# Kernel tuning notes

Hardware: AMD Instinct MI355X
Metric: run time of the kernel (lower is better)

The kernel has to match this reference:

```python
import jax, jax.numpy as jnp
import numpy as np

V, E, H, L, B = 32004, 512, 512, 128, 64  # vocab(+4), emb, hidden, seq_len, batch


def setup_inputs() -> dict:
    key = jax.random.key(0)
    ks = jax.random.split(key, 8)
    emb = jax.random.normal(ks[0], (V, E), jnp.float32) * 0.02
    emb = emb.at[0].set(0.0)  # padding_idx = PAD = 0
    Wx_f = jax.random.normal(ks[1], (E, 3 * H), jnp.float32) * 0.05
    Wh_f = jax.random.normal(ks[2], (H, 3 * H), jnp.float32) * 0.05
    b_f = jnp.zeros((3 * H,), jnp.float32)
    Wx_b = jax.random.normal(ks[3], (E, 3 * H), jnp.float32) * 0.05
    Wh_b = jax.random.normal(ks[4], (H, 3 * H), jnp.float32) * 0.05
    b_b = jnp.zeros((3 * H,), jnp.float32)
    xs = jax.random.randint(ks[5], (L, B), 0, V)
    xs_mask = jnp.ones((L, B), jnp.float32)
    return {"xs": xs, "xs_mask": xs_mask, "emb": emb,
            "Wx_f": Wx_f, "Wh_f": Wh_f, "b_f": b_f,
            "Wx_b": Wx_b, "Wh_b": Wh_b, "b_b": b_b}


def _gru_scan(xs_e, mask, Wx, Wh, b, reverse):
    # Precompute all input-to-gate projections in one big GEMM: [L,B,3H]
    xw = jnp.einsum('lbe,eg->lbg', xs_e, Wx) + b

    def step(h, inp):
        xw_t, m = inp                       # [B,3H], [B]
        hw = h @ Wh                         # [B,3H]
        xz, xr, xh = jnp.split(xw_t, 3, -1)
        hz, hr, hh = jnp.split(hw, 3, -1)
        z = jax.nn.sigmoid(xz + hz)
        r = jax.nn.sigmoid(xr + hr)
        h_tilde = jnp.tanh(xh + r * hh)
        h_new = (1.0 - z) * h + z * h_tilde
        m = m[:, None]
        h_new = m * h_new + (1.0 - m) * h   # masked timesteps keep previous state
        return h_new, h_new

    h0 = jnp.zeros((xs_e.shape[1], Wh.shape[0]), xs_e.dtype)
    _, hs = jax.lax.scan(step, h0, (xw, mask), reverse=reverse)
    return hs  # [L,B,H], time-ordered (reverse=True already yields original order)


def reference(xs, xs_mask, emb, Wx_f, Wh_f, b_f, Wx_b, Wh_b, b_b):
    xs_e = emb[xs]                                   # [L,B,E]
    right = _gru_scan(xs_e, xs_mask, Wx_f, Wh_f, b_f, reverse=False)
    left = _gru_scan(xs_e, xs_mask, Wx_b, Wh_b, b_b, reverse=True)
    r1 = jnp.concatenate([right, left], axis=-1)      # [L,B,2H]
    r2 = left[0]                                      # final backward state (after t=0)
    return r1, r2
```

## Files before the change

kernel.cpp:

```cpp
#include <hip/hip_runtime.h>
#include <stdint.h>

typedef _Float16 f16;
typedef _Float16 f16x8 __attribute__((ext_vector_type(8)));
typedef float    f32x4 __attribute__((ext_vector_type(4)));
typedef unsigned long long u64;

#define L_    128
#define B_    64
#define E_    512
#define H_    512
#define G3    1536
#define NCOL  3072

__device__ __forceinline__ float sigm_(float x){ return 1.0f/(1.0f + __expf(-x)); }
__device__ __forceinline__ float tanh_(float x){ return 1.0f - 2.0f/(__expf(2.0f*x) + 1.0f); }

__global__ __launch_bounds__(256) void k_zero(uint4* flags){
  flags[(size_t)blockIdx.x*256 + threadIdx.x] = make_uint4(0,0,0,0);
}

__global__ __launch_bounds__(256) void k_embed(const int* __restrict__ xs,
                                               const float* __restrict__ emb,
                                               f16* __restrict__ Xe){
  int row = blockIdx.x*2 + (threadIdx.x >> 7);
  int c   = (threadIdx.x & 127) * 4;
  int idx = xs[row];
  float4 v = *(const float4*)(emb + (size_t)idx*E_ + c);
  union { f16 h[4]; uint2 u; } p;
  p.h[0] = (f16)v.x; p.h[1] = (f16)v.y; p.h[2] = (f16)v.z; p.h[3] = (f16)v.w;
  *(uint2*)(Xe + (size_t)row*E_ + c) = p.u;
}

__global__ __launch_bounds__(256) void k_transpose(const float* __restrict__ Wx_f, const float* __restrict__ Wx_b,
                                                   const float* __restrict__ Wh_f, const float* __restrict__ Wh_b,
                                                   f16* __restrict__ WxT, f16* __restrict__ WhT){
  int mat = blockIdx.z;
  const float* src = mat==0 ? Wx_f : mat==1 ? Wx_b : mat==2 ? Wh_f : Wh_b;
  f16* dst = (mat < 2) ? (WxT + (size_t)mat*G3*E_) : (WhT + (size_t)(mat-2)*G3*H_);
  int n0 = blockIdx.x*64, k0 = blockIdx.y*64;
  __shared__ f16 tile[64][65];
  int tid = threadIdx.x;
  for (int i=0;i<16;i++){
    int r = i*4 + (tid>>6);
    int c = tid & 63;
    tile[r][c] = (f16)src[(size_t)(k0+r)*G3 + n0 + c];
  }
  __syncthreads();
  for (int i=0;i<16;i++){
    int n = i*4 + (tid>>6);
    int k = tid & 63;
    dst[(size_t)(n0+n)*512 + k0 + k] = tile[k][n];
  }
}

__global__ __launch_bounds__(256) void k_gemm(const f16* __restrict__ Xe, const f16* __restrict__ WxT,
                                              const float* __restrict__ bf, const float* __restrict__ bb,
                                              f16* __restrict__ xw2){
  __shared__ __align__(16) f16 sA[128*32];
  __shared__ __align__(16) f16 sB[128*32];
  const int tid = threadIdx.x;
  const int l = tid & 63, w = tid >> 6;
  const int wr = w >> 1, wc = w & 1;
  const int m0 = blockIdx.y*128, n0 = blockIdx.x*128;
  const int rl = l & 15, sg = l >> 4;
  f32x4 acc[4][4] = {};
  for (int kk=0; kk<16; ++kk){
    __syncthreads();
    for (int i=0;i<2;i++){
      int c = i*256 + tid; int row = c>>2, s = c&3;
      int sw = s ^ ((row>>1)&3);
      *(uint4*)&sA[row*32 + sw*8] = *(const uint4*)(Xe  + (size_t)(m0+row)*512 + kk*32 + s*8);
      *(uint4*)&sB[row*32 + sw*8] = *(const uint4*)(WxT + (size_t)(n0+row)*512 + kk*32 + s*8);
    }
    __syncthreads();
    f16x8 a[4], b[4];
    for (int mi=0;mi<4;mi++){ int m=(wr*4+mi)*16+rl; a[mi] = *(const f16x8*)&sA[m*32 + ((sg^((m>>1)&3))*8)]; }
    for (int nj=0;nj<4;nj++){ int n=(wc*4+nj)*16+rl; b[nj] = *(const f16x8*)&sB[n*32 + ((sg^((n>>1)&3))*8)]; }
    for (int mi=0;mi<4;mi++)
      for (int nj=0;nj<4;nj++)
        acc[mi][nj] = __builtin_amdgcn_mfma_f32_16x16x32_f16(a[mi], b[nj], acc[mi][nj], 0,0,0);
  }
  for (int nj=0;nj<4;nj++){
    int n = n0 + (wc*4+nj)*16 + rl;
    float bias = (n < G3) ? bf[n] : bb[n-G3];
    for (int mi=0;mi<4;mi++){
      int sub = (wr*4+mi)*16 + sg*4;
      int t   = (m0 + sub) >> 6;
      int b0  = sub & 63;
      union { f16 h[4]; uint2 u; } p;
      for (int r=0;r<4;r++) p.h[r] = (f16)(acc[mi][nj][r] + bias);
      *(uint2*)(xw2 + ((size_t)t*NCOL + n)*B_ + b0) = p.u;
    }
  }
}

__global__ __launch_bounds__(256, 1) void k_scan(const f16* __restrict__ xw2, const f16* __restrict__ WhT,
                                                 f16* __restrict__ hbuf, const float* __restrict__ mask,
                                                 float* __restrict__ out, unsigned* __restrict__ flags){
  const int dir = blockIdx.x >> 5, g = blockIdx.x & 31;
  __shared__ __align__(16) f16 sW[48*512];
  __shared__ __align__(16) f16 sX[4*16*16];
  const int tid = threadIdx.x, l = tid & 63, wv = tid >> 6;
  {
    const f16* base = WhT + (size_t)dir*G3*512;
    int cs = tid & 15;
    for (int r = tid>>4; r < 48; r += 16){
      int rowg = (r>>4)*512 + g*16 + (r&15);
      const uint4* src = (const uint4*)(base + (size_t)rowg*512);
      for (int j=0;j<4;j++){
        int s = cs*4 + j;
        *(uint4*)&sW[r*512 + ((s^(r&7))*8)] = src[s];
      }
    }
  }
  const int fl = l & 15, sg = l >> 4;
  const int mb   = wv*16 + sg*4;
  const int arow = wv*16 + fl;
  const int swz  = fl & 7;
  __syncthreads();
  f16x8 pz[16], pr[16], ph[16];
  #pragma unroll
  for (int kk=0;kk<16;kk++){
    int s = kk*4 + sg;
    pz[kk] = *(const f16x8*)&sW[(     fl)*512 + ((s^swz)*8)];
    pr[kk] = *(const f16x8*)&sW[(16 + fl)*512 + ((s^swz)*8)];
    ph[kk] = *(const f16x8*)&sW[(32 + fl)*512 + ((s^swz)*8)];
  }
  #pragma unroll
  for (int kk=0;kk<16;kk++){
    asm volatile("" : "+v"(pz[kk]));
    asm volatile("" : "+v"(pr[kk]));
    asm volatile("" : "+v"(ph[kk]));
  }
  float hstate[4] = {0.f,0.f,0.f,0.f};
  float* out2 = out + (size_t)L_*B_*1024;
  unsigned* myflag = flags + (size_t)(dir*32 + g)*32;
  const unsigned* pollp = flags + (size_t)dir*1024 + (size_t)(l&31)*32;
  f16* const sXw = &sX[wv*256];
  const int prow = l >> 2, pf = (l & 3)*4;

  for (int ti=0; ti<128; ++ti){
    const int t = dir ? (127 - ti) : ti;
    size_t xb = ((size_t)t*NCOL + dir*G3 + g*16 + fl)*B_ + mb;
    union { uint2 u; f16 h[4]; } xzv, xrv, xhv;
    xzv.u = *(const uint2*)(xw2 + xb);
    xrv.u = *(const uint2*)(xw2 + xb + (size_t)512*B_);
    xhv.u = *(const uint2*)(xw2 + xb + (size_t)1024*B_);
    float4 mv4 = *(const float4*)(mask + t*B_ + mb);
    f32x4 az = {0,0,0,0}, ar = {0,0,0,0}, ah = {0,0,0,0};
    if (ti){
      unsigned tgt = (unsigned)ti;
      while (true){
        unsigned f = __hip_atomic_load(pollp, __ATOMIC_RELAXED, __HIP_MEMORY_SCOPE_AGENT);
        if (__all((int)(f >= tgt))) break;
      }
      const u64* hq = (const u64*)(hbuf + ((size_t)dir*2 + (ti&1))*(64*512)) + (size_t)arow*128;
      u64 q[32];
      #pragma unroll
      for (int kk=0;kk<16;kk++){
        int j = kk*8 + sg*2;
        q[2*kk  ] = __hip_atomic_load(hq + j,     __ATOMIC_RELAXED, __HIP_MEMORY_SCOPE_AGENT);
        q[2*kk+1] = __hip_atomic_load(hq + j + 1, __ATOMIC_RELAXED, __HIP_MEMORY_SCOPE_AGENT);
      }
      #pragma unroll
      for (int kk=0;kk<16;kk++){
        union { u64 d[2]; f16x8 h; } a;
        a.d[0] = q[2*kk]; a.d[1] = q[2*kk+1];
        az = __builtin_amdgcn_mfma_f32_16x16x32_f16(a.h, pz[kk], az, 0,0,0);
        ar = __builtin_amdgcn_mfma_f32_16x16x32_f16(a.h, pr[kk], ar, 0,0,0);
        ah = __builtin_amdgcn_mfma_f32_16x16x32_f16(a.h, ph[kk], ah, 0,0,0);
      }
    }
    #pragma unroll
    for (int r=0;r<4;r++){
      float z  = sigm_((float)xzv.h[r] + az[r]);
      float rr = sigm_((float)xrv.h[r] + ar[r]);
      float ht = tanh_((float)xhv.h[r] + rr*ah[r]);
      float mv = (&mv4.x)[r];
      float hn = (1.0f - z)*hstate[r] + z*ht;
      hn = mv*hn + (1.0f - mv)*hstate[r];
      hstate[r] = hn;
    }
    if (ti < 127){
      #pragma unroll
      for (int r=0;r<4;r++) sXw[(sg*4 + r)*16 + fl] = (f16)hstate[r];
      asm volatile("s_waitcnt lgkmcnt(0)" ::: "memory");
      u64 v = *(const u64*)&sXw[prow*16 + pf];
      f16* hb = hbuf + ((size_t)dir*2 + ((ti&1)^1))*(64*512);
      __hip_atomic_store((u64*)(hb + (size_t)(wv*16 + prow)*512 + g*16 + pf), v,
                         __ATOMIC_RELAXED, __HIP_MEMORY_SCOPE_AGENT);
      __syncthreads();
      if (tid == 0)
        __hip_atomic_store(myflag, (unsigned)(ti+1),
                           __ATOMIC_RELAXED, __HIP_MEMORY_SCOPE_AGENT);
    }
    #pragma unroll
    for (int r=0;r<4;r++){
      int m = mb + r;
      out[((size_t)(t*B_+m))*1024 + dir*512 + g*16 + fl] = hstate[r];
    }
    if (dir==1 && t==0){
      #pragma unroll
      for (int r=0;r<4;r++)
        out2[(size_t)(mb+r)*512 + g*16 + fl] = hstate[r];
    }
  }
}

extern "C" void kernel_launch(void* const* d_in, const int* in_sizes, int n_in,
                              void* d_out, int out_size, void* d_ws, size_t ws_size,
                              hipStream_t stream){
  const int*   xs      = (const int*)  d_in[0];
  const float* xs_mask = (const float*)d_in[1];
  const float* emb     = (const float*)d_in[2];
  const float* Wx_f    = (const float*)d_in[3];
  const float* Wh_f    = (const float*)d_in[4];
  const float* b_f     = (const float*)d_in[5];
  const float* Wx_b    = (const float*)d_in[6];
  const float* Wh_b    = (const float*)d_in[7];
  const float* b_b     = (const float*)d_in[8];

  char* w = (char*)d_ws;
  f16*      Xe    = (f16*)(w);
  f16*      WxT   = (f16*)(w + 8388608);
  f16*      WhT   = (f16*)(w + 11534336);
  f16*      xw2   = (f16*)(w + 14680064);
  f16*      hbuf  = (f16*)(w + 65011712);
  unsigned* flags = (unsigned*)(w + 65273856);
  float*    out   = (float*)d_out;

  k_zero     <<<dim3(2),       dim3(256), 0, stream>>>((uint4*)flags);
  k_embed    <<<dim3(4096),    dim3(256), 0, stream>>>(xs, emb, Xe);
  k_transpose<<<dim3(24,8,4),  dim3(256), 0, stream>>>(Wx_f, Wx_b, Wh_f, Wh_b, WxT, WhT);
  k_gemm     <<<dim3(24,64),   dim3(256), 0, stream>>>(Xe, WxT, b_f, b_b, xw2);
  k_scan     <<<dim3(64),      dim3(256), 0, stream>>>(xw2, WhT, hbuf, xs_mask, out, flags);
}
```

Baseline: 731.3 us.

## Replace per-block flags with timestep tags embedded in fp32 hidden-state words

Removes the separate flag array, the barrier and the flag store. Each block now publishes its hidden state as fp32 values whose low 13 mantissa bits carry the timestep tag, so consumers spin on the data itself and retry until every word carries the expected tag. This takes the __syncthreads-then-flag round trip off the recurrent critical path. In exchange it doubles the hidden-state traffic, adds a tag check and repack on every load, and reuses the WxT workspace region, which is zeroed after the GEMM has consumed it.

```diff
diff --git a/kernel.cpp b/kernel.cpp
--- a/kernel.cpp
+++ b/kernel.cpp
@@ -16,8 +16,8 @@
 __device__ __forceinline__ float sigm_(float x){ return 1.0f/(1.0f + __expf(-x)); }
 __device__ __forceinline__ float tanh_(float x){ return 1.0f - 2.0f/(__expf(2.0f*x) + 1.0f); }
 
-__global__ __launch_bounds__(256) void k_zero(uint4* flags){
-  flags[(size_t)blockIdx.x*256 + threadIdx.x] = make_uint4(0,0,0,0);
+__global__ __launch_bounds__(256) void k_zero(uint4* hb){
+  hb[(size_t)blockIdx.x*256 + threadIdx.x] = make_uint4(0,0,0,0);
 }
 
 __global__ __launch_bounds__(256) void k_embed(const int* __restrict__ xs,
@@ -96,11 +96,11 @@
 }
 
 __global__ __launch_bounds__(256, 1) void k_scan(const f16* __restrict__ xw2, const f16* __restrict__ WhT,
-                                                 f16* __restrict__ hbuf, const float* __restrict__ mask,
-                                                 float* __restrict__ out, unsigned* __restrict__ flags){
+                                                 float* __restrict__ hbuf32, const float* __restrict__ mask,
+                                                 float* __restrict__ out){
   const int dir = blockIdx.x >> 5, g = blockIdx.x & 31;
-  __shared__ __align__(16) f16 sW[48*512];
-  __shared__ __align__(16) f16 sX[4*16*16];
+  __shared__ __align__(16) f16   sW[48*512];
+  __shared__ __align__(16) float sX[4*16*16];
   const int tid = threadIdx.x, l = tid & 63, wv = tid >> 6;
   {
     const f16* base = WhT + (size_t)dir*G3*512;
@@ -135,9 +135,7 @@
   }
   float hstate[4] = {0.f,0.f,0.f,0.f};
   float* out2 = out + (size_t)L_*B_*1024;
-  unsigned* myflag = flags + (size_t)(dir*32 + g)*32;
-  const unsigned* pollp = flags + (size_t)dir*1024 + (size_t)(l&31)*32;
-  f16* const sXw = &sX[wv*256];
+  float* const sXw = &sX[wv*256];
   const int prow = l >> 2, pf = (l & 3)*4;
 
   for (int ti=0; ti<128; ++ti){
@@ -150,26 +148,54 @@
     float4 mv4 = *(const float4*)(mask + t*B_ + mb);
     f32x4 az = {0,0,0,0}, ar = {0,0,0,0}, ah = {0,0,0,0};
     if (ti){
-      unsigned tgt = (unsigned)ti;
-      while (true){
-        unsigned f = __hip_atomic_load(pollp, __ATOMIC_RELAXED, __HIP_MEMORY_SCOPE_AGENT);
-        if (__all((int)(f >= tgt))) break;
+      const unsigned tag = (unsigned)ti;
+      const u64* hq = (const u64*)hbuf32 + (size_t)(dir*2 + (ti&1))*16384;
+      const size_t rowb = (size_t)arow*256;
+      {
+        const u64* sp = hq + rowb + (size_t)(l&31)*8;
+        while (true){
+          u64 s = __hip_atomic_load(sp, __ATOMIC_RELAXED, __HIP_MEMORY_SCOPE_AGENT);
+          if (__all((int)((((unsigned)s ^ tag) & 0x1FFFu) == 0u))) break;
+        }
       }
-      const u64* hq = (const u64*)(hbuf + ((size_t)dir*2 + (ti&1))*(64*512)) + (size_t)arow*128;
-      u64 q[32];
+      f16x8 fr[16];
+      unsigned mism;
+      do {
+        mism = 0u;
+        #pragma unroll
+        for (int kk=0;kk<16;kk++){
+          const u64* p = hq + rowb + (size_t)((kk*4+sg)*4);
+          u64 q0 = __hip_atomic_load(p,   __ATOMIC_RELAXED, __HIP_MEMORY_SCOPE_AGENT);
+          u64 q1 = __hip_atomic_load(p+1, __ATOMIC_RELAXED, __HIP_MEMORY_SCOPE_AGENT);
+          u64 q2 = __hip_atomic_load(p+2, __ATOMIC_RELAXED, __HIP_MEMORY_SCOPE_AGENT);
+          u64 q3 = __hip_atomic_load(p+3, __ATOMIC_RELAXED, __HIP_MEMORY_SCOPE_AGENT);
+          mism |= ((unsigned)q0 ^ tag) | ((unsigned)q1 ^ tag)
+                | ((unsigned)q2 ^ tag) | ((unsigned)q3 ^ tag);
+          union { float f; unsigned u; } e0, o0;
+          union { f16x8 v; unsigned uu[4]; } fb;
+          union { _Float16 h2[2]; unsigned u; } pk;
+          e0.u = (unsigned)q0 & ~0x1FFFu; o0.u = (unsigned)(q0 >> 32);
+          pk.h2[0] = (_Float16)0;
+          { auto c = __builtin_amdgcn_cvt_pkrtz(e0.f, o0.f); pk.h2[0]=c[0]; pk.h2[1]=c[1]; }
+          fb.uu[0] = pk.u;
+          e0.u = (unsigned)q1 & ~0x1FFFu; o0.u = (unsigned)(q1 >> 32);
+          { auto c = __builtin_amdgcn_cvt_pkrtz(e0.f, o0.f); pk.h2[0]=c[0]; pk.h2[1]=c[1]; }
+          fb.uu[1] = pk.u;
+          e0.u = (unsigned)q2 & ~0x1FFFu; o0.u = (unsigned)(q2 >> 32);
+          { auto c = __builtin_amdgcn_cvt_pkrtz(e0.f, o0.f); pk.h2[0]=c[0]; pk.h2[1]=c[1]; }
+          fb.uu[2] = pk.u;
+          e0.u = (unsigned)q3 & ~0x1FFFu; o0.u = (unsigned)(q3 >> 32);
+          { auto c = __builtin_amdgcn_cvt_pkrtz(e0.f, o0.f); pk.h2[0]=c[0]; pk.h2[1]=c[1]; }
+          fb.uu[3] = pk.u;
+          fr[kk] = fb.v;
+        }
+        mism &= 0x1FFFu;
+      } while (!__all((int)(mism == 0u)));
       #pragma unroll
       for (int kk=0;kk<16;kk++){
-        int j = kk*8 + sg*2;
-        q[2*kk  ] = __hip_atomic_load(hq + j,     __ATOMIC_RELAXED, __HIP_MEMORY_SCOPE_AGENT);
-        q[2*kk+1] = __hip_atomic_load(hq + j + 1, __ATOMIC_RELAXED, __HIP_MEMORY_SCOPE_AGENT);
-      }
-      #pragma unroll
-      for (int kk=0;kk<16;kk++){
-        union { u64 d[2]; f16x8 h; } a;
-        a.d[0] = q[2*kk]; a.d[1] = q[2*kk+1];
-        az = __builtin_amdgcn_mfma_f32_16x16x32_f16(a.h, pz[kk], az, 0,0,0);
-        ar = __builtin_amdgcn_mfma_f32_16x16x32_f16(a.h, pr[kk], ar, 0,0,0);
-        ah = __builtin_amdgcn_mfma_f32_16x16x32_f16(a.h, ph[kk], ah, 0,0,0);
+        az = __builtin_amdgcn_mfma_f32_16x16x32_f16(fr[kk], pz[kk], az, 0,0,0);
+        ar = __builtin_amdgcn_mfma_f32_16x16x32_f16(fr[kk], pr[kk], ar, 0,0,0);
+        ah = __builtin_amdgcn_mfma_f32_16x16x32_f16(fr[kk], ph[kk], ah, 0,0,0);
       }
     }
     #pragma unroll
@@ -184,16 +210,18 @@
     }
     if (ti < 127){
       #pragma unroll
-      for (int r=0;r<4;r++) sXw[(sg*4 + r)*16 + fl] = (f16)hstate[r];
+      for (int r=0;r<4;r++) sXw[(sg*4 + r)*16 + fl] = (float)(f16)hstate[r];
       asm volatile("s_waitcnt lgkmcnt(0)" ::: "memory");
-      u64 v = *(const u64*)&sXw[prow*16 + pf];
-      f16* hb = hbuf + ((size_t)dir*2 + ((ti&1)^1))*(64*512);
-      __hip_atomic_store((u64*)(hb + (size_t)(wv*16 + prow)*512 + g*16 + pf), v,
-                         __ATOMIC_RELAXED, __HIP_MEMORY_SCOPE_AGENT);
-      __syncthreads();
-      if (tid == 0)
-        __hip_atomic_store(myflag, (unsigned)(ti+1),
-                           __ATOMIC_RELAXED, __HIP_MEMORY_SCOPE_AGENT);
+      float4 tv = *(const float4*)&sXw[prow*16 + pf];
+      const unsigned tg = (unsigned)(ti + 1);
+      union { float f; unsigned u; } a0,a1,a2,a3;
+      a0.f = tv.x; a1.f = tv.y; a2.f = tv.z; a3.f = tv.w;
+      u64 w0 = (u64)(a0.u | tg) | ((u64)a1.u << 32);
+      u64 w1 = (u64)(a2.u | tg) | ((u64)a3.u << 32);
+      u64* hb = (u64*)hbuf32 + (size_t)(dir*2 + ((ti&1)^1))*16384
+              + (size_t)(wv*16 + prow)*256 + g*8 + (pf>>1);
+      __hip_atomic_store(hb,   w0, __ATOMIC_RELAXED, __HIP_MEMORY_SCOPE_AGENT);
+      __hip_atomic_store(hb+1, w1, __ATOMIC_RELAXED, __HIP_MEMORY_SCOPE_AGENT);
     }
     #pragma unroll
     for (int r=0;r<4;r++){
@@ -222,17 +250,16 @@
   const float* b_b     = (const float*)d_in[8];
 
   char* w = (char*)d_ws;
-  f16*      Xe    = (f16*)(w);
-  f16*      WxT   = (f16*)(w + 8388608);
-  f16*      WhT   = (f16*)(w + 11534336);
-  f16*      xw2   = (f16*)(w + 14680064);
-  f16*      hbuf  = (f16*)(w + 65011712);
-  unsigned* flags = (unsigned*)(w + 65273856);
-  float*    out   = (float*)d_out;
-
-  k_zero     <<<dim3(2),       dim3(256), 0, stream>>>((uint4*)flags);
+  f16*   Xe     = (f16*)(w);
+  f16*   WxT    = (f16*)(w + 8388608);
+  float* hbuf32 = (float*)(w + 8388608);
+  f16*   WhT    = (f16*)(w + 11534336);
+  f16*   xw2    = (f16*)(w + 14680064);
+  float* out    = (float*)d_out;
+
   k_embed    <<<dim3(4096),    dim3(256), 0, stream>>>(xs, emb, Xe);
   k_transpose<<<dim3(24,8,4),  dim3(256), 0, stream>>>(Wx_f, Wx_b, Wh_f, Wh_b, WxT, WhT);
   k_gemm     <<<dim3(24,64),   dim3(256), 0, stream>>>(Xe, WxT, b_f, b_b, xw2);
-  k_scan     <<<dim3(64),      dim3(256), 0, stream>>>(xw2, WhT, hbuf, xs_mask, out, flags);
-}
+  k_zero     <<<dim3(128),     dim3(256), 0, stream>>>((uint4*)hbuf32);
+  k_scan     <<<dim3(64),      dim3(256), 0, stream>>>(xw2, WhT, hbuf32, xs_mask, out);
+}
```

After: 1.301 ms. 1.78x slower.

## Halve scan workgroups to 32, each owning 32 hidden units per direction

Applied to the files above, without the earlier changes.

The recurrent scan now uses 16 workgroups per direction instead of 32, each handling 32 hidden columns. The recurrent weights are no longer held in registers; each step reads them from a larger LDS tile, doing twice the MFMA work per workgroup. The aim is to cut the number of workgroups that must synchronise through global flags each step and to shrink polling fan-in. The cost is more serial work per step and per-step LDS reads of the weights.

```diff
diff --git a/kernel.cpp b/kernel.cpp
--- a/kernel.cpp
+++ b/kernel.cpp
@@ -12,12 +12,14 @@
 #define H_    512
 #define G3    1536
 #define NCOL  3072
+#define NGRP  16
 
 __device__ __forceinline__ float sigm_(float x){ return 1.0f/(1.0f + __expf(-x)); }
 __device__ __forceinline__ float tanh_(float x){ return 1.0f - 2.0f/(__expf(2.0f*x) + 1.0f); }
 
-__global__ __launch_bounds__(256) void k_zero(uint4* flags){
-  flags[(size_t)blockIdx.x*256 + threadIdx.x] = make_uint4(0,0,0,0);
+__global__ __launch_bounds__(256) void k_zero(unsigned* p){
+  p[threadIdx.x*4+0] = 0u; p[threadIdx.x*4+1] = 0u;
+  p[threadIdx.x*4+2] = 0u; p[threadIdx.x*4+3] = 0u;
 }
 
 __global__ __launch_bounds__(256) void k_embed(const int* __restrict__ xs,
@@ -98,15 +100,15 @@
 __global__ __launch_bounds__(256, 1) void k_scan(const f16* __restrict__ xw2, const f16* __restrict__ WhT,
                                                  f16* __restrict__ hbuf, const float* __restrict__ mask,
                                                  float* __restrict__ out, unsigned* __restrict__ flags){
-  const int dir = blockIdx.x >> 5, g = blockIdx.x & 31;
-  __shared__ __align__(16) f16 sW[48*512];
-  __shared__ __align__(16) f16 sX[4*16*16];
+  const int dir = blockIdx.x >> 4, g16 = blockIdx.x & 15;
+  __shared__ __align__(16) f16 sW[96*512];
+  __shared__ __align__(16) f16 sX[4*16*32];
   const int tid = threadIdx.x, l = tid & 63, wv = tid >> 6;
   {
     const f16* base = WhT + (size_t)dir*G3*512;
     int cs = tid & 15;
-    for (int r = tid>>4; r < 48; r += 16){
-      int rowg = (r>>4)*512 + g*16 + (r&15);
+    for (int r = tid>>4; r < 96; r += 16){
+      int rowg = (r>>5)*512 + g16*32 + (r&31);
       const uint4* src = (const uint4*)(base + (size_t)rowg*512);
       for (int j=0;j<4;j++){
         int s = cs*4 + j;
@@ -117,38 +119,25 @@
   const int fl = l & 15, sg = l >> 4;
   const int mb   = wv*16 + sg*4;
   const int arow = wv*16 + fl;
-  const int swz  = fl & 7;
   __syncthreads();
-  f16x8 pz[16], pr[16], ph[16];
-  #pragma unroll
-  for (int kk=0;kk<16;kk++){
-    int s = kk*4 + sg;
-    pz[kk] = *(const f16x8*)&sW[(     fl)*512 + ((s^swz)*8)];
-    pr[kk] = *(const f16x8*)&sW[(16 + fl)*512 + ((s^swz)*8)];
-    ph[kk] = *(const f16x8*)&sW[(32 + fl)*512 + ((s^swz)*8)];
-  }
-  #pragma unroll
-  for (int kk=0;kk<16;kk++){
-    asm volatile("" : "+v"(pz[kk]));
-    asm volatile("" : "+v"(pr[kk]));
-    asm volatile("" : "+v"(ph[kk]));
-  }
-  float hstate[4] = {0.f,0.f,0.f,0.f};
+  float hstate[2][4] = {};
   float* out2 = out + (size_t)L_*B_*1024;
-  unsigned* myflag = flags + (size_t)(dir*32 + g)*32;
-  const unsigned* pollp = flags + (size_t)dir*1024 + (size_t)(l&31)*32;
-  f16* const sXw = &sX[wv*256];
-  const int prow = l >> 2, pf = (l & 3)*4;
+  unsigned* myflag = flags + (size_t)(dir*16 + g16)*32;
+  const unsigned* pollp = flags + (size_t)dir*512 + (size_t)(l&15)*32;
+  f16* const sXw = &sX[wv*512];
+  const int prow = l >> 2, pf = (l & 3)*8;
 
   for (int ti=0; ti<128; ++ti){
     const int t = dir ? (127 - ti) : ti;
-    size_t xb = ((size_t)t*NCOL + dir*G3 + g*16 + fl)*B_ + mb;
-    union { uint2 u; f16 h[4]; } xzv, xrv, xhv;
-    xzv.u = *(const uint2*)(xw2 + xb);
-    xrv.u = *(const uint2*)(xw2 + xb + (size_t)512*B_);
-    xhv.u = *(const uint2*)(xw2 + xb + (size_t)1024*B_);
+    size_t xbase = ((size_t)t*NCOL + dir*G3 + g16*32 + fl)*B_ + mb;
+    union { uint2 u; f16 h[4]; } xg[3][2];
+    #pragma unroll
+    for (int gt=0; gt<3; ++gt)
+      #pragma unroll
+      for (int hf=0; hf<2; ++hf)
+        xg[gt][hf].u = *(const uint2*)(xw2 + xbase + ((size_t)gt*512 + hf*16)*B_);
     float4 mv4 = *(const float4*)(mask + t*B_ + mb);
-    f32x4 az = {0,0,0,0}, ar = {0,0,0,0}, ah = {0,0,0,0};
+    f32x4 acc[3][2] = {};
     if (ti){
       unsigned tgt = (unsigned)ti;
       while (true){
@@ -167,43 +156,58 @@
       for (int kk=0;kk<16;kk++){
         union { u64 d[2]; f16x8 h; } a;
         a.d[0] = q[2*kk]; a.d[1] = q[2*kk+1];
-        az = __builtin_amdgcn_mfma_f32_16x16x32_f16(a.h, pz[kk], az, 0,0,0);
-        ar = __builtin_amdgcn_mfma_f32_16x16x32_f16(a.h, pr[kk], ar, 0,0,0);
-        ah = __builtin_amdgcn_mfma_f32_16x16x32_f16(a.h, ph[kk], ah, 0,0,0);
+        int s = kk*4 + sg;
+        #pragma unroll
+        for (int gt=0; gt<3; ++gt)
+          #pragma unroll
+          for (int hf=0; hf<2; ++hf){
+            int rr = gt*32 + hf*16 + fl;
+            f16x8 b = *(const f16x8*)&sW[rr*512 + ((s^(rr&7))*8)];
+            acc[gt][hf] = __builtin_amdgcn_mfma_f32_16x16x32_f16(a.h, b, acc[gt][hf], 0,0,0);
+          }
       }
     }
     #pragma unroll
-    for (int r=0;r<4;r++){
-      float z  = sigm_((float)xzv.h[r] + az[r]);
-      float rr = sigm_((float)xrv.h[r] + ar[r]);
-      float ht = tanh_((float)xhv.h[r] + rr*ah[r]);
-      float mv = (&mv4.x)[r];
-      float hn = (1.0f - z)*hstate[r] + z*ht;
-      hn = mv*hn + (1.0f - mv)*hstate[r];
-      hstate[r] = hn;
-    }
+    for (int hf=0; hf<2; ++hf)
+      #pragma unroll
+      for (int r=0;r<4;r++){
+        float z  = sigm_((float)xg[0][hf].h[r] + acc[0][hf][r]);
+        float rr = sigm_((float)xg[1][hf].h[r] + acc[1][hf][r]);
+        float ht = tanh_((float)xg[2][hf].h[r] + rr*acc[2][hf][r]);
+        float mv = (&mv4.x)[r];
+        float hn = (1.0f - z)*hstate[hf][r] + z*ht;
+        hn = mv*hn + (1.0f - mv)*hstate[hf][r];
+        hstate[hf][r] = hn;
+      }
     if (ti < 127){
       #pragma unroll
-      for (int r=0;r<4;r++) sXw[(sg*4 + r)*16 + fl] = (f16)hstate[r];
+      for (int hf=0; hf<2; ++hf)
+        #pragma unroll
+        for (int r=0;r<4;r++)
+          sXw[(sg*4 + r)*32 + hf*16 + fl] = (f16)hstate[hf][r];
       asm volatile("s_waitcnt lgkmcnt(0)" ::: "memory");
-      u64 v = *(const u64*)&sXw[prow*16 + pf];
-      f16* hb = hbuf + ((size_t)dir*2 + ((ti&1)^1))*(64*512);
-      __hip_atomic_store((u64*)(hb + (size_t)(wv*16 + prow)*512 + g*16 + pf), v,
-                         __ATOMIC_RELAXED, __HIP_MEMORY_SCOPE_AGENT);
+      u64 v0 = *(const u64*)&sXw[prow*32 + pf];
+      u64 v1 = *(const u64*)&sXw[prow*32 + pf + 4];
+      f16* hb = hbuf + ((size_t)dir*2 + ((ti&1)^1))*(64*512)
+              + (size_t)(wv*16 + prow)*512 + g16*32 + pf;
+      __hip_atomic_store((u64*)hb,     v0, __ATOMIC_RELAXED, __HIP_MEMORY_SCOPE_AGENT);
+      __hip_atomic_store((u64*)hb + 1, v1, __ATOMIC_RELAXED, __HIP_MEMORY_SCOPE_AGENT);
       __syncthreads();
       if (tid == 0)
         __hip_atomic_store(myflag, (unsigned)(ti+1),
                            __ATOMIC_RELAXED, __HIP_MEMORY_SCOPE_AGENT);
     }
     #pragma unroll
-    for (int r=0;r<4;r++){
-      int m = mb + r;
-      out[((size_t)(t*B_+m))*1024 + dir*512 + g*16 + fl] = hstate[r];
-    }
+    for (int hf=0; hf<2; ++hf)
+      #pragma unroll
+      for (int r=0;r<4;r++)
+        out[((size_t)(t*B_+mb+r))*1024 + dir*512 + g16*32 + hf*16 + fl] = hstate[hf][r];
     if (dir==1 && t==0){
       #pragma unroll
-      for (int r=0;r<4;r++)
-        out2[(size_t)(mb+r)*512 + g*16 + fl] = hstate[r];
+      for (int hf=0; hf<2; ++hf)
+        #pragma unroll
+        for (int r=0;r<4;r++)
+          out2[(size_t)(mb+r)*512 + g16*32 + hf*16 + fl] = hstate[hf][r];
     }
   }
 }
@@ -230,9 +234,9 @@
   unsigned* flags = (unsigned*)(w + 65273856);
   float*    out   = (float*)d_out;
 
-  k_zero     <<<dim3(2),       dim3(256), 0, stream>>>((uint4*)flags);
+  k_zero     <<<dim3(1),       dim3(256), 0, stream>>>(flags);
   k_embed    <<<dim3(4096),    dim3(256), 0, stream>>>(xs, emb, Xe);
   k_transpose<<<dim3(24,8,4),  dim3(256), 0, stream>>>(Wx_f, Wx_b, Wh_f, Wh_b, WxT, WhT);
   k_gemm     <<<dim3(24,64),   dim3(256), 0, stream>>>(Xe, WxT, b_f, b_b, xw2);
-  k_scan     <<<dim3(64),      dim3(256), 0, stream>>>(xw2, WhT, hbuf, xs_mask, out, flags);
-}
+  k_scan     <<<dim3(32),      dim3(256), 0, stream>>>(xw2, WhT, hbuf, xs_mask, out, flags);
+}
```

Result: slower. 928.1 us (+26.9%).

## Process recurrent matmul in chunks as producer flags arrive; fold flag zeroing into embed

Applied to the files above, without the earlier changes.

The scan's per-step wait for every producer block to publish its hidden-state slice now uses partial-readiness tracking. Each lane polls its producer's flag and a ballot builds a readiness mask. The 16 K-steps of the recurrent MFMA are split into 4 chunks of 128 hidden columns (one group of 8 lanes per chunk), and each chunk is computed as soon as its 8 producer flags are ready instead of after a full barrier. The separate flag-zeroing kernel is also merged into the embedding kernel's first block, saving one launch. The cost is more complex control flow: a switch over macro-expanded chunks that may affect register use, and in-order chunk processing that still stalls on the earliest unready chunk.

```diff
diff --git a/kernel.cpp b/kernel.cpp
--- a/kernel.cpp
+++ b/kernel.cpp
@@ -16,13 +16,14 @@
 __device__ __forceinline__ float sigm_(float x){ return 1.0f/(1.0f + __expf(-x)); }
 __device__ __forceinline__ float tanh_(float x){ return 1.0f - 2.0f/(__expf(2.0f*x) + 1.0f); }
 
-__global__ __launch_bounds__(256) void k_zero(uint4* flags){
-  flags[(size_t)blockIdx.x*256 + threadIdx.x] = make_uint4(0,0,0,0);
-}
-
 __global__ __launch_bounds__(256) void k_embed(const int* __restrict__ xs,
                                                const float* __restrict__ emb,
-                                               f16* __restrict__ Xe){
+                                               f16* __restrict__ Xe,
+                                               uint4* __restrict__ flags4){
+  if (blockIdx.x == 0){
+    flags4[threadIdx.x]       = make_uint4(0,0,0,0);
+    flags4[256 + threadIdx.x] = make_uint4(0,0,0,0);
+  }
   int row = blockIdx.x*2 + (threadIdx.x >> 7);
   int c   = (threadIdx.x & 127) * 4;
   int idx = xs[row];
@@ -150,26 +151,65 @@
     float4 mv4 = *(const float4*)(mask + t*B_ + mb);
     f32x4 az = {0,0,0,0}, ar = {0,0,0,0}, ah = {0,0,0,0};
     if (ti){
-      unsigned tgt = (unsigned)ti;
-      while (true){
-        unsigned f = __hip_atomic_load(pollp, __ATOMIC_RELAXED, __HIP_MEMORY_SCOPE_AGENT);
-        if (__all((int)(f >= tgt))) break;
-      }
+      const unsigned tgt = (unsigned)ti;
       const u64* hq = (const u64*)(hbuf + ((size_t)dir*2 + (ti&1))*(64*512)) + (size_t)arow*128;
-      u64 q[32];
-      #pragma unroll
-      for (int kk=0;kk<16;kk++){
-        int j = kk*8 + sg*2;
-        q[2*kk  ] = __hip_atomic_load(hq + j,     __ATOMIC_RELAXED, __HIP_MEMORY_SCOPE_AGENT);
-        q[2*kk+1] = __hip_atomic_load(hq + j + 1, __ATOMIC_RELAXED, __HIP_MEMORY_SCOPE_AGENT);
-      }
-      #pragma unroll
-      for (int kk=0;kk<16;kk++){
-        union { u64 d[2]; f16x8 h; } a;
-        a.d[0] = q[2*kk]; a.d[1] = q[2*kk+1];
-        az = __builtin_amdgcn_mfma_f32_16x16x32_f16(a.h, pz[kk], az, 0,0,0);
-        ar = __builtin_amdgcn_mfma_f32_16x16x32_f16(a.h, pr[kk], ar, 0,0,0);
-        ah = __builtin_amdgcn_mfma_f32_16x16x32_f16(a.h, ph[kk], ah, 0,0,0);
+      unsigned f = __hip_atomic_load(pollp, __ATOMIC_RELAXED, __HIP_MEMORY_SCOPE_AGENT);
+      u64 bal = __ballot((int)(f >= tgt));
+      if (bal == ~0ull){
+        u64 q[32];
+        #pragma unroll
+        for (int kk=0;kk<16;kk++){
+          int j = kk*8 + sg*2;
+          q[2*kk  ] = __hip_atomic_load(hq + j,     __ATOMIC_RELAXED, __HIP_MEMORY_SCOPE_AGENT);
+          q[2*kk+1] = __hip_atomic_load(hq + j + 1, __ATOMIC_RELAXED, __HIP_MEMORY_SCOPE_AGENT);
+        }
+        #pragma unroll
+        for (int kk=0;kk<16;kk++){
+          union { u64 d[2]; f16x8 h; } a;
+          a.d[0] = q[2*kk]; a.d[1] = q[2*kk+1];
+          az = __builtin_amdgcn_mfma_f32_16x16x32_f16(a.h, pz[kk], az, 0,0,0);
+          ar = __builtin_amdgcn_mfma_f32_16x16x32_f16(a.h, pr[kk], ar, 0,0,0);
+          ah = __builtin_amdgcn_mfma_f32_16x16x32_f16(a.h, ph[kk], ah, 0,0,0);
+        }
+      } else {
+        #define CHUNK(C)                                                                   \
+        {                                                                                  \
+          u64 q[8];                                                                        \
+          _Pragma("unroll")                                                                \
+          for (int k=0;k<4;k++){                                                           \
+            int j = ((C)*4 + k)*8 + sg*2;                                                  \
+            q[2*k  ] = __hip_atomic_load(hq + j,     __ATOMIC_RELAXED, __HIP_MEMORY_SCOPE_AGENT); \
+            q[2*k+1] = __hip_atomic_load(hq + j + 1, __ATOMIC_RELAXED, __HIP_MEMORY_SCOPE_AGENT); \
+          }                                                                                \
+          _Pragma("unroll")                                                                \
+          for (int k=0;k<4;k++){                                                           \
+            union { u64 d[2]; f16x8 h; } a;                                                \
+            a.d[0] = q[2*k]; a.d[1] = q[2*k+1];                                            \
+            az = __builtin_amdgcn_mfma_f32_16x16x32_f16(a.h, pz[(C)*4+k], az, 0,0,0);      \
+            ar = __builtin_amdgcn_mfma_f32_16x16x32_f16(a.h, pr[(C)*4+k], ar, 0,0,0);      \
+            ah = __builtin_amdgcn_mfma_f32_16x16x32_f16(a.h, ph[(C)*4+k], ah, 0,0,0);      \
+          }                                                                                \
+        }
+        int cur = 0;
+        unsigned m = (unsigned)bal;
+        while (cur < 4){
+          int nxt = cur;
+          while (nxt < 4 && ((m >> (8*nxt)) & 0xFFu) == 0xFFu) ++nxt;
+          for (int c = cur; c < nxt; ++c){
+            switch (c){
+              case 0: CHUNK(0); break;
+              case 1: CHUNK(1); break;
+              case 2: CHUNK(2); break;
+              default: CHUNK(3); break;
+            }
+          }
+          cur = nxt;
+          if (cur < 4){
+            f = __hip_atomic_load(pollp, __ATOMIC_RELAXED, __HIP_MEMORY_SCOPE_AGENT);
+            m = (unsigned)__ballot((int)(f >= tgt));
+          }
+        }
+        #undef CHUNK
       }
     }
     #pragma unroll
@@ -230,8 +270,7 @@
   unsigned* flags = (unsigned*)(w + 65273856);
   float*    out   = (float*)d_out;
 
-  k_zero     <<<dim3(2),       dim3(256), 0, stream>>>((uint4*)flags);
-  k_embed    <<<dim3(4096),    dim3(256), 0, stream>>>(xs, emb, Xe);
+  k_embed    <<<dim3(4096),    dim3(256), 0, stream>>>(xs, emb, Xe, (uint4*)flags);
   k_transpose<<<dim3(24,8,4),  dim3(256), 0, stream>>>(Wx_f, Wx_b, Wh_f, Wh_b, WxT, WhT);
   k_gemm     <<<dim3(24,64),   dim3(256), 0, stream>>>(Xe, WxT, b_f, b_b, xw2);
   k_scan     <<<dim3(64),      dim3(256), 0, stream>>>(xw2, WhT, hbuf, xs_mask, out, flags);
```

Measured after the change: 803.6 us. 9.9% more time.
